# Performance work log

Measured on AMD Instinct MI355X. Metric: run time of the kernel, lower is better.

Reference implementation:

```python
import jax, jax.numpy as jnp
import numpy as np

N = 20000
E = 640000
D = 128


def setup_inputs() -> dict:
    key = jax.random.key(0)
    ks = jax.random.split(key, 8)
    x = jax.random.normal(ks[0], (N, D), dtype=jnp.float32)
    edge_index = jax.random.randint(ks[1], (2, E), 0, N, dtype=jnp.int64)
    s = 1.0 / np.sqrt(D)
    inp = {"x": x, "edge_index": edge_index}
    for i, layer in enumerate([2, 4, 6]):
        inp[f"W{i+1}"] = jax.random.uniform(ks[layer], (D, D), jnp.float32, -s, s)
        inp[f"b{i+1}"] = jax.random.uniform(ks[layer + 1], (D,), jnp.float32, -s, s)
    return inp


def _gcn_layer(x, src, dst, deg_inv, W, b):
    # linear (torch convention: y = x @ W.T + b), W: [out, in]
    xt = x @ W.T + b
    # gather source-node features, scatter-mean onto targets
    msg = xt[src]                                   # [E, D]
    agg = jax.ops.segment_sum(msg, dst, num_segments=N)  # [N, D]
    agg = agg * deg_inv[:, None]                    # mean over incoming edges
    return jax.nn.relu(agg) + xt


def reference(x, edge_index, W1, b1, W2, b2, W3, b3):
    src, dst = edge_index[0], edge_index[1]
    deg = jax.ops.segment_sum(jnp.ones((E,), jnp.float32), dst, num_segments=N)
    deg_inv = jnp.where(deg > 0, 1.0 / jnp.maximum(deg, 1.0), 0.0)
    for W, b in ((W1, b1), (W2, b2), (W3, b3)):
        x = _gcn_layer(x, src, dst, deg_inv, W, b)
    return x
```

## Files before the change

### kernel.cpp

```cpp
#include <hip/hip_runtime.h>

#define DD 128
#define KC 32
#define MT 64
#define ELLC 128
#define NBMAX 320
#define ACAP 2304
#define AEPW 4096

__device__ __forceinline__ unsigned f2bf_rne(float f) {
    unsigned u = __float_as_uint(f);
    u += 0x7fffu + ((u >> 16) & 1u);
    return u >> 16;
}

__device__ __forceinline__ void gemm_body(float Xs[KC][MT + 4], float Ws[KC][DD + 4],
                                          const float* x,
                                          const float* __restrict__ W,
                                          const float* __restrict__ b,
                                          float* xt,
                                          unsigned* __restrict__ xtb, int M, int PS, int blk) {
    const int tid  = threadIdx.x;
    const int cg   = tid & 15;
    const int rg   = tid >> 4;
    const int row0 = blk * MT;

    float acc[4][8];
#pragma unroll
    for (int i = 0; i < 4; ++i)
#pragma unroll
        for (int j = 0; j < 8; ++j) acc[i][j] = 0.0f;

    for (int kc = 0; kc < DD; kc += KC) {
#pragma unroll
        for (int it = 0; it < 2; ++it) {
            int idx = tid + it * 256;
            int r = idx >> 3, kq = idx & 7;
            int gr = row0 + r;
            float4 v = make_float4(0.f, 0.f, 0.f, 0.f);
            if (gr < M) v = *(const float4*)&x[gr * DD + kc + kq * 4];
            Xs[kq * 4 + 0][r] = v.x; Xs[kq * 4 + 1][r] = v.y;
            Xs[kq * 4 + 2][r] = v.z; Xs[kq * 4 + 3][r] = v.w;
        }
#pragma unroll
        for (int it = 0; it < 4; ++it) {
            int idx = tid + it * 256;
            int o = idx >> 3, kq = idx & 7;
            float4 v = *(const float4*)&W[o * DD + kc + kq * 4];
            Ws[kq * 4 + 0][o] = v.x; Ws[kq * 4 + 1][o] = v.y;
            Ws[kq * 4 + 2][o] = v.z; Ws[kq * 4 + 3][o] = v.w;
        }
        __syncthreads();

#pragma unroll 8
        for (int k = 0; k < KC; ++k) {
            float4 xv = *(const float4*)&Xs[k][rg * 4];
            float4 w0 = *(const float4*)&Ws[k][cg * 8];
            float4 w1 = *(const float4*)&Ws[k][cg * 8 + 4];
            float xr[4] = {xv.x, xv.y, xv.z, xv.w};
            float wc[8] = {w0.x, w0.y, w0.z, w0.w, w1.x, w1.y, w1.z, w1.w};
#pragma unroll
            for (int i = 0; i < 4; ++i)
#pragma unroll
                for (int j = 0; j < 8; ++j) acc[i][j] += xr[i] * wc[j];
        }
        __syncthreads();
    }

    float4 b0 = *(const float4*)&b[cg * 8];
    float4 b1 = *(const float4*)&b[cg * 8 + 4];
    float bb[8] = {b0.x, b0.y, b0.z, b0.w, b1.x, b1.y, b1.z, b1.w};
#pragma unroll
    for (int i = 0; i < 4; ++i) {
        int gr = row0 + rg * 4 + i;
        if (gr < M) {
            float v[8];
#pragma unroll
            for (int j = 0; j < 8; ++j) v[j] = acc[i][j] + bb[j];
            *(float4*)&xt[gr * DD + cg * 8]     = make_float4(v[0], v[1], v[2], v[3]);
            *(float4*)&xt[gr * DD + cg * 8 + 4] = make_float4(v[4], v[5], v[6], v[7]);
            uint4 p;
            p.x = f2bf_rne(v[0]) | (f2bf_rne(v[1]) << 16);
            p.y = f2bf_rne(v[2]) | (f2bf_rne(v[3]) << 16);
            p.z = f2bf_rne(v[4]) | (f2bf_rne(v[5]) << 16);
            p.w = f2bf_rne(v[6]) | (f2bf_rne(v[7]) << 16);
            unsigned* xp = xtb + (size_t)(cg >> 3) * ((size_t)PS * 32)
                               + (size_t)gr * 32 + ((cg & 7) << 2);
            *(uint4*)xp = p;
        }
    }
}

__global__ __launch_bounds__(256) void gemm_xwT(const float* x,
                                                const float* __restrict__ W,
                                                const float* __restrict__ b,
                                                float* xt,
                                                unsigned* __restrict__ xtb, int M, int PS) {
    __shared__ float Xs[KC][MT + 4];
    __shared__ float Ws[KC][DD + 4];
    gemm_body(Xs, Ws, x, W, b, xt, xtb, M, PS, blockIdx.x);
}

__global__ __launch_bounds__(256) void gemm1_plus_binA(const float* x,
                                                       const float* __restrict__ W,
                                                       const float* __restrict__ b,
                                                       float* xt,
                                                       unsigned* __restrict__ xtb, int M, int PS,
                                                       const int* __restrict__ src,
                                                       const int* __restrict__ dst,
                                                       int* __restrict__ bucket_count,
                                                       unsigned* __restrict__ bstore,
                                                       int E, int NB, int PA) {
    __shared__ float Xs[KC][MT + 4];
    __shared__ float Ws[KC][DD + 4];
    __shared__ int hist[NBMAX];
    __shared__ int basec[NBMAX];
    __shared__ int cur[NBMAX];

    if ((int)blockIdx.x >= PA) {
        gemm_body(Xs, Ws, x, W, b, xt, xtb, M, PS, blockIdx.x - PA);
        return;
    }

    const int tid = threadIdx.x;
    for (int i = tid; i < NB; i += 256) hist[i] = 0;
    __syncthreads();

    int dv[16], sv[16];
    const int ebase = blockIdx.x * AEPW;
#pragma unroll
    for (int r = 0; r < 4; ++r) {
        int e = ebase + r * 1024 + tid * 4;
        if (e + 4 <= E) {
            int4 d4 = *(const int4*)&dst[e];
            int4 s4 = *(const int4*)&src[e];
            dv[r*4+0] = d4.x; dv[r*4+1] = d4.y; dv[r*4+2] = d4.z; dv[r*4+3] = d4.w;
            sv[r*4+0] = s4.x; sv[r*4+1] = s4.y; sv[r*4+2] = s4.z; sv[r*4+3] = s4.w;
        } else {
#pragma unroll
            for (int q = 0; q < 4; ++q) {
                int ee = e + q;
                if (ee < E) { dv[r*4+q] = dst[ee]; sv[r*4+q] = src[ee]; }
                else        { dv[r*4+q] = -1;      sv[r*4+q] = 0; }
            }
        }
    }
#pragma unroll
    for (int i = 0; i < 16; ++i)
        if (dv[i] >= 0) atomicAdd(&hist[dv[i] >> 6], 1);
    __syncthreads();

    for (int bk = tid; bk < NB; bk += 256) {
        int h = hist[bk];
        basec[bk] = h ? atomicAdd(&bucket_count[bk], h) : 0;
        cur[bk] = 0;
    }
    __syncthreads();

#pragma unroll
    for (int i = 0; i < 16; ++i) {
        if (dv[i] >= 0) {
            int bk = dv[i] >> 6;
            int pos = basec[bk] + atomicAdd(&cur[bk], 1);
            if (pos < ACAP)
                bstore[bk * ACAP + pos] = ((unsigned)(dv[i] & 63) << 16) | (unsigned)sv[i];
        }
    }
}

__global__ __launch_bounds__(256) void ell_build(const unsigned* __restrict__ bstore,
                                                 const int* __restrict__ bucket_count,
                                                 unsigned short* __restrict__ colell,
                                                 int* __restrict__ deg,
                                                 unsigned* __restrict__ xtb,
                                                 int PS, int N) {
    __shared__ int c64[64];
    const int bk = blockIdx.x;
    for (int i = threadIdx.x; i < 64; i += 256) c64[i] = 0;
    __syncthreads();
    int cnt = bucket_count[bk];
    if (cnt > ACAP) cnt = ACAP;
    for (int i = threadIdx.x; i < cnt; i += 256) {
        unsigned code = bstore[bk * ACAP + i];
        int local = (int)(code >> 16);
        int s     = (int)(code & 0xffffu);
        int p = atomicAdd(&c64[local], 1);
        if (p < ELLC)
            colell[((((bk << 6) + local)) << 7) + p] = (unsigned short)s;
    }
    __syncthreads();
    if (threadIdx.x < 64) {
        int node = (bk << 6) + threadIdx.x;
        if (node < N) {
            int d = c64[threadIdx.x];
            deg[node] = d;
            int stored = d < ELLC ? d : ELLC;
            int padded = (stored + 15) & ~15;
            if (padded > ELLC) padded = ELLC;
            unsigned short* row = colell + ((size_t)node << 7);
            for (int p2 = stored; p2 < padded; ++p2) row[p2] = (unsigned short)N;
        }
    }
    if (bk == 0 && threadIdx.x >= 64 && threadIdx.x < 80) {
        int i  = threadIdx.x - 64;
        int pl = i >> 3;
        int j  = i & 7;
        *(uint4*)&xtb[((size_t)pl * PS + (size_t)N) * 32 + (size_t)j * 4] =
            make_uint4(0u, 0u, 0u, 0u);
    }
}

__global__ __launch_bounds__(256) void gcn_aggregate(const uint2* __restrict__ xtb2,
                                                     const float* xt,
                                                     const unsigned short* __restrict__ colell,
                                                     const int* __restrict__ deg,
                                                     float* out, int PS, int N) {
    const int wave  = threadIdx.x >> 6;
    const int lane  = threadIdx.x & 63;
    const int xcd   = blockIdx.x & 7;
    const int plane = xcd >> 2;
    const int widx  = ((blockIdx.x >> 3) << 2) | (xcd & 3);
    const int node  = (widx << 2) | wave;
    if (node >= N) return;
    const int h = lane & 15;
    const int q = lane >> 4;

    const uint2* __restrict__ xl = xtb2 + (size_t)plane * ((size_t)PS << 4) + h;
    const unsigned short* __restrict__ crow = colell + ((size_t)node << 7);
    const int cnt = deg[node];
    const int cl  = cnt < ELLC ? cnt : ELLC;

    float a0 = 0.f, a1 = 0.f, a2 = 0.f, a3 = 0.f;

#define GATH(u_, j_) { int s_ = __shfl(myidx, ((t + (j_)) << 2) | q, 64); \
                       (u_)[j_] = xl[(size_t)s_ << 4]; }
#define UNPK(u_, j_) { a0 += __uint_as_float((u_)[j_].x << 16); \
                       a1 += __uint_as_float((u_)[j_].x & 0xffff0000u); \
                       a2 += __uint_as_float((u_)[j_].y << 16); \
                       a3 += __uint_as_float((u_)[j_].y & 0xffff0000u); }

    for (int base = 0; base < cl; base += 64) {
        const int rem = cl - base;
        const int c = rem < 64 ? rem : 64;
        const int myidx = (int)crow[base + lane];
        const int cq = ((c + 15) >> 4) << 2;
        int t = 0;
        for (; t + 8 <= cq; t += 8) {
            uint2 u[8];
            GATH(u,0) GATH(u,1) GATH(u,2) GATH(u,3)
            GATH(u,4) GATH(u,5) GATH(u,6) GATH(u,7)
            UNPK(u,0) UNPK(u,1) UNPK(u,2) UNPK(u,3)
            UNPK(u,4) UNPK(u,5) UNPK(u,6) UNPK(u,7)
        }
        if (t < cq) {
            uint2 u[4];
            GATH(u,0) GATH(u,1) GATH(u,2) GATH(u,3)
            UNPK(u,0) UNPK(u,1) UNPK(u,2) UNPK(u,3)
        }
    }
#undef GATH
#undef UNPK

    a0 += __shfl_down(a0, 32, 64);
    a1 += __shfl_down(a1, 32, 64);
    a2 += __shfl_down(a2, 32, 64);
    a3 += __shfl_down(a3, 32, 64);
    a0 += __shfl_down(a0, 16, 64);
    a1 += __shfl_down(a1, 16, 64);
    a2 += __shfl_down(a2, 16, 64);
    a3 += __shfl_down(a3, 16, 64);

    if (q == 0) {
        const float di = (cnt > 0) ? (1.0f / (float)cnt) : 0.0f;
        float4 t4 = ((const float4*)xt)[(size_t)node * 32 + plane * 16 + h];
        float4 o;
        o.x = fmaxf(a0 * di, 0.f) + t4.x;
        o.y = fmaxf(a1 * di, 0.f) + t4.y;
        o.z = fmaxf(a2 * di, 0.f) + t4.z;
        o.w = fmaxf(a3 * di, 0.f) + t4.w;
        ((float4*)out)[(size_t)node * 32 + plane * 16 + h] = o;
    }
}

extern "C" void kernel_launch(void* const* d_in, const int* in_sizes, int n_in,
                              void* d_out, int out_size, void* d_ws, size_t ws_size,
                              hipStream_t stream) {
    const float* x  = (const float*)d_in[0];
    const int*   ei = (const int*)d_in[1];
    const float* W1 = (const float*)d_in[2];
    const float* b1 = (const float*)d_in[3];
    const float* W2 = (const float*)d_in[4];
    const float* b2 = (const float*)d_in[5];
    const float* W3 = (const float*)d_in[6];
    const float* b3 = (const float*)d_in[7];

    const int N  = in_sizes[0] / DD;
    const int E  = in_sizes[1] / 2;
    const int PS = N + 1;

    const int* src = ei;
    const int* dst = ei + E;

    const int NB = (N + 63) >> 6;
    const int PA = (E + AEPW - 1) / AEPW;
    const int GB = (N + MT - 1) / MT;
    const int SUP = (N + 15) >> 4;
    const int AGB = SUP * 8;

    char* ws = (char*)d_ws;
    size_t off = 0;
    auto alloc = [&](size_t bytes) {
        void* p = ws + off;
        off += (bytes + 255) & ~(size_t)255;
        return p;
    };
    int*            bucket_count = (int*)alloc((size_t)NB * sizeof(int));
    unsigned*       bstore       = (unsigned*)alloc((size_t)NB * ACAP * sizeof(unsigned));
    unsigned short* colell       = (unsigned short*)alloc((size_t)NB * 64 * ELLC * sizeof(unsigned short));
    int*            deg          = (int*)alloc((size_t)N * sizeof(int));
    unsigned*       xtb          = (unsigned*)alloc((size_t)PS * 256);

    float* xbuf = (float*)d_out;

    hipMemsetAsync(bucket_count, 0, (size_t)NB * sizeof(int), stream);
    gemm1_plus_binA<<<PA + GB, 256, 0, stream>>>(x, W1, b1, xbuf, xtb, N, PS,
                                                 src, dst, bucket_count, bstore, E, NB, PA);
    ell_build<<<NB, 256, 0, stream>>>(bstore, bucket_count, colell, deg, xtb, PS, N);

    gcn_aggregate<<<AGB, 256, 0, stream>>>((const uint2*)xtb, xbuf, colell, deg, xbuf, PS, N);

    gemm_xwT<<<GB, 256, 0, stream>>>(xbuf, W2, b2, xbuf, xtb, N, PS);
    gcn_aggregate<<<AGB, 256, 0, stream>>>((const uint2*)xtb, xbuf, colell, deg, xbuf, PS, N);

    gemm_xwT<<<GB, 256, 0, stream>>>(xbuf, W3, b3, xbuf, xtb, N, PS);
    gcn_aggregate<<<AGB, 256, 0, stream>>>((const uint2*)xtb, xbuf, colell, deg, xbuf, PS, N);
}
```

Before: 213.5 us.

## Use persistent work-queue aggregation with XCC-aware plane assignment and finer padding

Replaces the static-grid aggregation kernel with a persistent kernel of fixed block count. Blocks grab groups of 16 nodes from per-plane atomic counters, first on the feature plane matched to their XCC, then help with the other plane. ELL row padding drops from multiples of 16 to multiples of 4, and a single-step gather tail replaces the 4-wide one, so fewer padding gathers are wasted. This costs atomic contention, two block syncs per chunk and a hardware-register read, and it relies on the XCC id to keep each plane's data local in cache.

```diff
diff --git a/kernel.cpp b/kernel.cpp
--- a/kernel.cpp
+++ b/kernel.cpp
@@ -7,6 +7,8 @@
 #define NBMAX 320
 #define ACAP 2304
 #define AEPW 4096
+#define AGB  1024
+#define QG   16
 
 __device__ __forceinline__ unsigned f2bf_rne(float f) {
     unsigned u = __float_as_uint(f);
@@ -14,14 +16,20 @@
     return u >> 16;
 }
 
-__device__ __forceinline__ void gemm_body(float Xs[KC][MT + 4], float Ws[KC][DD + 4],
+__device__ __forceinline__ int xcc_id() {
+    unsigned v;
+    asm volatile("s_getreg_b32 %0, hwreg(20, 0, 4)" : "=s"(v));
+    return (int)(v & 7u);
+}
+
+__device__ __forceinline__ void gemm_body(float (*Xs)[MT + 4], float (*Ws)[DD + 4],
                                           const float* x,
                                           const float* __restrict__ W,
                                           const float* __restrict__ b,
                                           float* xt,
                                           unsigned* __restrict__ xtb, int M, int PS, int blk) {
     const int tid  = threadIdx.x;
-    const int cg   = tid & 15;
+    const int cg_  = tid & 15;
     const int rg   = tid >> 4;
     const int row0 = blk * MT;
 
@@ -55,8 +63,8 @@
 #pragma unroll 8
         for (int k = 0; k < KC; ++k) {
             float4 xv = *(const float4*)&Xs[k][rg * 4];
-            float4 w0 = *(const float4*)&Ws[k][cg * 8];
-            float4 w1 = *(const float4*)&Ws[k][cg * 8 + 4];
+            float4 w0 = *(const float4*)&Ws[k][cg_ * 8];
+            float4 w1 = *(const float4*)&Ws[k][cg_ * 8 + 4];
             float xr[4] = {xv.x, xv.y, xv.z, xv.w};
             float wc[8] = {w0.x, w0.y, w0.z, w0.w, w1.x, w1.y, w1.z, w1.w};
 #pragma unroll
@@ -67,8 +75,8 @@
         __syncthreads();
     }
 
-    float4 b0 = *(const float4*)&b[cg * 8];
-    float4 b1 = *(const float4*)&b[cg * 8 + 4];
+    float4 b0 = *(const float4*)&b[cg_ * 8];
+    float4 b1 = *(const float4*)&b[cg_ * 8 + 4];
     float bb[8] = {b0.x, b0.y, b0.z, b0.w, b1.x, b1.y, b1.z, b1.w};
 #pragma unroll
     for (int i = 0; i < 4; ++i) {
@@ -77,15 +85,15 @@
             float v[8];
 #pragma unroll
             for (int j = 0; j < 8; ++j) v[j] = acc[i][j] + bb[j];
-            *(float4*)&xt[gr * DD + cg * 8]     = make_float4(v[0], v[1], v[2], v[3]);
-            *(float4*)&xt[gr * DD + cg * 8 + 4] = make_float4(v[4], v[5], v[6], v[7]);
+            *(float4*)&xt[gr * DD + cg_ * 8]     = make_float4(v[0], v[1], v[2], v[3]);
+            *(float4*)&xt[gr * DD + cg_ * 8 + 4] = make_float4(v[4], v[5], v[6], v[7]);
             uint4 p;
             p.x = f2bf_rne(v[0]) | (f2bf_rne(v[1]) << 16);
             p.y = f2bf_rne(v[2]) | (f2bf_rne(v[3]) << 16);
             p.z = f2bf_rne(v[4]) | (f2bf_rne(v[5]) << 16);
             p.w = f2bf_rne(v[6]) | (f2bf_rne(v[7]) << 16);
-            unsigned* xp = xtb + (size_t)(cg >> 3) * ((size_t)PS * 32)
-                               + (size_t)gr * 32 + ((cg & 7) << 2);
+            unsigned* xp = xtb + (size_t)(cg_ >> 3) * ((size_t)PS * 32)
+                               + (size_t)gr * 32 + ((cg_ & 7) << 2);
             *(uint4*)xp = p;
         }
     }
@@ -110,6 +118,7 @@
                                                        const int* __restrict__ dst,
                                                        int* __restrict__ bucket_count,
                                                        unsigned* __restrict__ bstore,
+                                                       int* __restrict__ qc,
                                                        int E, int NB, int PA) {
     __shared__ float Xs[KC][MT + 4];
     __shared__ float Ws[KC][DD + 4];
@@ -123,6 +132,7 @@
     }
 
     const int tid = threadIdx.x;
+    if (blockIdx.x == 0 && tid < 6) qc[tid] = 0;
     for (int i = tid; i < NB; i += 256) hist[i] = 0;
     __syncthreads();
 
@@ -195,7 +205,7 @@
             int d = c64[threadIdx.x];
             deg[node] = d;
             int stored = d < ELLC ? d : ELLC;
-            int padded = (stored + 15) & ~15;
+            int padded = (stored + 3) & ~3;
             if (padded > ELLC) padded = ELLC;
             unsigned short* row = colell + ((size_t)node << 7);
             for (int p2 = stored; p2 < padded; ++p2) row[p2] = (unsigned short)N;
@@ -210,18 +220,10 @@
     }
 }
 
-__global__ __launch_bounds__(256) void gcn_aggregate(const uint2* __restrict__ xtb2,
-                                                     const float* xt,
-                                                     const unsigned short* __restrict__ colell,
-                                                     const int* __restrict__ deg,
-                                                     float* out, int PS, int N) {
-    const int wave  = threadIdx.x >> 6;
-    const int lane  = threadIdx.x & 63;
-    const int xcd   = blockIdx.x & 7;
-    const int plane = xcd >> 2;
-    const int widx  = ((blockIdx.x >> 3) << 2) | (xcd & 3);
-    const int node  = (widx << 2) | wave;
-    if (node >= N) return;
+__device__ __forceinline__ void agg_one(const uint2* __restrict__ xtb2, const float* xt,
+                                        const unsigned short* __restrict__ colell,
+                                        const int* __restrict__ deg, float* out,
+                                        int PS, int node, int plane, int lane) {
     const int h = lane & 15;
     const int q = lane >> 4;
 
@@ -243,7 +245,7 @@
         const int rem = cl - base;
         const int c = rem < 64 ? rem : 64;
         const int myidx = (int)crow[base + lane];
-        const int cq = ((c + 15) >> 4) << 2;
+        const int cq = (c + 3) >> 2;
         int t = 0;
         for (; t + 8 <= cq; t += 8) {
             uint2 u[8];
@@ -252,10 +254,9 @@
             UNPK(u,0) UNPK(u,1) UNPK(u,2) UNPK(u,3)
             UNPK(u,4) UNPK(u,5) UNPK(u,6) UNPK(u,7)
         }
-        if (t < cq) {
-            uint2 u[4];
-            GATH(u,0) GATH(u,1) GATH(u,2) GATH(u,3)
-            UNPK(u,0) UNPK(u,1) UNPK(u,2) UNPK(u,3)
+        for (; t < cq; ++t) {
+            uint2 u1[1];
+            GATH(u1,0) UNPK(u1,0)
         }
     }
 #undef GATH
@@ -279,6 +280,37 @@
         o.z = fmaxf(a2 * di, 0.f) + t4.z;
         o.w = fmaxf(a3 * di, 0.f) + t4.w;
         ((float4*)out)[(size_t)node * 32 + plane * 16 + h] = o;
+    }
+}
+
+__global__ __launch_bounds__(256) void gcn_aggregate_q(const uint2* __restrict__ xtb2,
+                                                       const float* xt,
+                                                       const unsigned short* __restrict__ colell,
+                                                       const int* __restrict__ deg,
+                                                       float* out,
+                                                       int* __restrict__ qc,
+                                                       int PS, int N) {
+    __shared__ int sbase;
+    const int wave = threadIdx.x >> 6;
+    const int lane = threadIdx.x & 63;
+    const int myplane = (xcc_id() >> 2) & 1;
+
+    for (int pass = 0; pass < 2; ++pass) {
+        const int plane = myplane ^ pass;
+        int* q = qc + plane;
+        for (;;) {
+            if (threadIdx.x == 0) sbase = atomicAdd(q, QG);
+            __syncthreads();
+            const int base = sbase;
+            __syncthreads();
+            if (base >= N) break;
+#pragma unroll
+            for (int r = 0; r < QG / 4; ++r) {
+                int node = base + (r << 2) + wave;
+                if (node < N)
+                    agg_one(xtb2, xt, colell, deg, out, PS, node, plane, lane);
+            }
+        }
     }
 }
 
@@ -304,8 +336,6 @@
     const int NB = (N + 63) >> 6;
     const int PA = (E + AEPW - 1) / AEPW;
     const int GB = (N + MT - 1) / MT;
-    const int SUP = (N + 15) >> 4;
-    const int AGB = SUP * 8;
 
     char* ws = (char*)d_ws;
     size_t off = 0;
@@ -319,19 +349,23 @@
     unsigned short* colell       = (unsigned short*)alloc((size_t)NB * 64 * ELLC * sizeof(unsigned short));
     int*            deg          = (int*)alloc((size_t)N * sizeof(int));
     unsigned*       xtb          = (unsigned*)alloc((size_t)PS * 256);
+    int*            qc           = (int*)alloc(6 * sizeof(int));
 
     float* xbuf = (float*)d_out;
 
     hipMemsetAsync(bucket_count, 0, (size_t)NB * sizeof(int), stream);
     gemm1_plus_binA<<<PA + GB, 256, 0, stream>>>(x, W1, b1, xbuf, xtb, N, PS,
-                                                 src, dst, bucket_count, bstore, E, NB, PA);
+                                                 src, dst, bucket_count, bstore, qc, E, NB, PA);
     ell_build<<<NB, 256, 0, stream>>>(bstore, bucket_count, colell, deg, xtb, PS, N);
 
-    gcn_aggregate<<<AGB, 256, 0, stream>>>((const uint2*)xtb, xbuf, colell, deg, xbuf, PS, N);
+    gcn_aggregate_q<<<AGB, 256, 0, stream>>>((const uint2*)xtb, xbuf, colell, deg, xbuf,
+                                             qc + 0, PS, N);
 
     gemm_xwT<<<GB, 256, 0, stream>>>(xbuf, W2, b2, xbuf, xtb, N, PS);
-    gcn_aggregate<<<AGB, 256, 0, stream>>>((const uint2*)xtb, xbuf, colell, deg, xbuf, PS, N);
+    gcn_aggregate_q<<<AGB, 256, 0, stream>>>((const uint2*)xtb, xbuf, colell, deg, xbuf,
+                                             qc + 2, PS, N);
 
     gemm_xwT<<<GB, 256, 0, stream>>>(xbuf, W3, b3, xbuf, xtb, N, PS);
-    gcn_aggregate<<<AGB, 256, 0, stream>>>((const uint2*)xtb, xbuf, colell, deg, xbuf, PS, N);
-}
+    gcn_aggregate_q<<<AGB, 256, 0, stream>>>((const uint2*)xtb, xbuf, colell, deg, xbuf,
+                                             qc + 4, PS, N);
+}
```

New measurement: 347.1 us. 62.6% more time.

## Process both feature planes per wave and shrink ELL padding to four

Applied to the files above, without the earlier changes.

The aggregate kernel now handles both 64-feature bf16 planes of a node in one wave, not splitting planes across XCD-mapped blocks. This halves the block count and reuses each shuffled neighbor index for two gathers. Row padding drops from 16 to 4 entries, and a scalar tail loop replaces the 4-wide remainder, so fewer dummy gathers are issued. The trade-off is losing the XCD-based plane locality for L2, which could make the gathers miss cache more often.

```diff
diff --git a/kernel.cpp b/kernel.cpp
--- a/kernel.cpp
+++ b/kernel.cpp
@@ -14,14 +14,14 @@
     return u >> 16;
 }
 
-__device__ __forceinline__ void gemm_body(float Xs[KC][MT + 4], float Ws[KC][DD + 4],
+__device__ __forceinline__ void gemm_body(float (*Xs)[MT + 4], float (*Ws)[DD + 4],
                                           const float* x,
                                           const float* __restrict__ W,
                                           const float* __restrict__ b,
                                           float* xt,
                                           unsigned* __restrict__ xtb, int M, int PS, int blk) {
     const int tid  = threadIdx.x;
-    const int cg   = tid & 15;
+    const int cg_  = tid & 15;
     const int rg   = tid >> 4;
     const int row0 = blk * MT;
 
@@ -55,8 +55,8 @@
 #pragma unroll 8
         for (int k = 0; k < KC; ++k) {
             float4 xv = *(const float4*)&Xs[k][rg * 4];
-            float4 w0 = *(const float4*)&Ws[k][cg * 8];
-            float4 w1 = *(const float4*)&Ws[k][cg * 8 + 4];
+            float4 w0 = *(const float4*)&Ws[k][cg_ * 8];
+            float4 w1 = *(const float4*)&Ws[k][cg_ * 8 + 4];
             float xr[4] = {xv.x, xv.y, xv.z, xv.w};
             float wc[8] = {w0.x, w0.y, w0.z, w0.w, w1.x, w1.y, w1.z, w1.w};
 #pragma unroll
@@ -67,8 +67,8 @@
         __syncthreads();
     }
 
-    float4 b0 = *(const float4*)&b[cg * 8];
-    float4 b1 = *(const float4*)&b[cg * 8 + 4];
+    float4 b0 = *(const float4*)&b[cg_ * 8];
+    float4 b1 = *(const float4*)&b[cg_ * 8 + 4];
     float bb[8] = {b0.x, b0.y, b0.z, b0.w, b1.x, b1.y, b1.z, b1.w};
 #pragma unroll
     for (int i = 0; i < 4; ++i) {
@@ -77,15 +77,15 @@
             float v[8];
 #pragma unroll
             for (int j = 0; j < 8; ++j) v[j] = acc[i][j] + bb[j];
-            *(float4*)&xt[gr * DD + cg * 8]     = make_float4(v[0], v[1], v[2], v[3]);
-            *(float4*)&xt[gr * DD + cg * 8 + 4] = make_float4(v[4], v[5], v[6], v[7]);
+            *(float4*)&xt[gr * DD + cg_ * 8]     = make_float4(v[0], v[1], v[2], v[3]);
+            *(float4*)&xt[gr * DD + cg_ * 8 + 4] = make_float4(v[4], v[5], v[6], v[7]);
             uint4 p;
             p.x = f2bf_rne(v[0]) | (f2bf_rne(v[1]) << 16);
             p.y = f2bf_rne(v[2]) | (f2bf_rne(v[3]) << 16);
             p.z = f2bf_rne(v[4]) | (f2bf_rne(v[5]) << 16);
             p.w = f2bf_rne(v[6]) | (f2bf_rne(v[7]) << 16);
-            unsigned* xp = xtb + (size_t)(cg >> 3) * ((size_t)PS * 32)
-                               + (size_t)gr * 32 + ((cg & 7) << 2);
+            unsigned* xp = xtb + (size_t)(cg_ >> 3) * ((size_t)PS * 32)
+                               + (size_t)gr * 32 + ((cg_ & 7) << 2);
             *(uint4*)xp = p;
         }
     }
@@ -195,7 +195,7 @@
             int d = c64[threadIdx.x];
             deg[node] = d;
             int stored = d < ELLC ? d : ELLC;
-            int padded = (stored + 15) & ~15;
+            int padded = (stored + 3) & ~3;
             if (padded > ELLC) padded = ELLC;
             unsigned short* row = colell + ((size_t)node << 7);
             for (int p2 = stored; p2 < padded; ++p2) row[p2] = (unsigned short)N;
@@ -215,70 +215,80 @@
                                                      const unsigned short* __restrict__ colell,
                                                      const int* __restrict__ deg,
                                                      float* out, int PS, int N) {
-    const int wave  = threadIdx.x >> 6;
-    const int lane  = threadIdx.x & 63;
-    const int xcd   = blockIdx.x & 7;
-    const int plane = xcd >> 2;
-    const int widx  = ((blockIdx.x >> 3) << 2) | (xcd & 3);
-    const int node  = (widx << 2) | wave;
+    const int wave = threadIdx.x >> 6;
+    const int lane = threadIdx.x & 63;
+    const int node = (int)blockIdx.x * 4 + wave;
     if (node >= N) return;
     const int h = lane & 15;
     const int q = lane >> 4;
 
-    const uint2* __restrict__ xl = xtb2 + (size_t)plane * ((size_t)PS << 4) + h;
+    const uint2* __restrict__ xl0 = xtb2 + h;
+    const uint2* __restrict__ xl1 = xtb2 + ((size_t)PS << 4) + h;
     const unsigned short* __restrict__ crow = colell + ((size_t)node << 7);
     const int cnt = deg[node];
     const int cl  = cnt < ELLC ? cnt : ELLC;
 
     float a0 = 0.f, a1 = 0.f, a2 = 0.f, a3 = 0.f;
-
-#define GATH(u_, j_) { int s_ = __shfl(myidx, ((t + (j_)) << 2) | q, 64); \
-                       (u_)[j_] = xl[(size_t)s_ << 4]; }
-#define UNPK(u_, j_) { a0 += __uint_as_float((u_)[j_].x << 16); \
-                       a1 += __uint_as_float((u_)[j_].x & 0xffff0000u); \
-                       a2 += __uint_as_float((u_)[j_].y << 16); \
-                       a3 += __uint_as_float((u_)[j_].y & 0xffff0000u); }
+    float a4 = 0.f, a5 = 0.f, a6 = 0.f, a7 = 0.f;
+
+#define GATH2(j_) { int s_ = __shfl(myidx, ((t + (j_)) << 2) | q, 64); \
+                    u0[j_] = xl0[(size_t)s_ << 4]; \
+                    u1[j_] = xl1[(size_t)s_ << 4]; }
+#define UNPK2(j_) { a0 += __uint_as_float(u0[j_].x << 16); \
+                    a1 += __uint_as_float(u0[j_].x & 0xffff0000u); \
+                    a2 += __uint_as_float(u0[j_].y << 16); \
+                    a3 += __uint_as_float(u0[j_].y & 0xffff0000u); \
+                    a4 += __uint_as_float(u1[j_].x << 16); \
+                    a5 += __uint_as_float(u1[j_].x & 0xffff0000u); \
+                    a6 += __uint_as_float(u1[j_].y << 16); \
+                    a7 += __uint_as_float(u1[j_].y & 0xffff0000u); }
 
     for (int base = 0; base < cl; base += 64) {
         const int rem = cl - base;
         const int c = rem < 64 ? rem : 64;
         const int myidx = (int)crow[base + lane];
-        const int cq = ((c + 15) >> 4) << 2;
+        const int cq = (c + 3) >> 2;
         int t = 0;
         for (; t + 8 <= cq; t += 8) {
-            uint2 u[8];
-            GATH(u,0) GATH(u,1) GATH(u,2) GATH(u,3)
-            GATH(u,4) GATH(u,5) GATH(u,6) GATH(u,7)
-            UNPK(u,0) UNPK(u,1) UNPK(u,2) UNPK(u,3)
-            UNPK(u,4) UNPK(u,5) UNPK(u,6) UNPK(u,7)
-        }
-        if (t < cq) {
-            uint2 u[4];
-            GATH(u,0) GATH(u,1) GATH(u,2) GATH(u,3)
-            UNPK(u,0) UNPK(u,1) UNPK(u,2) UNPK(u,3)
-        }
-    }
-#undef GATH
-#undef UNPK
-
-    a0 += __shfl_down(a0, 32, 64);
-    a1 += __shfl_down(a1, 32, 64);
-    a2 += __shfl_down(a2, 32, 64);
-    a3 += __shfl_down(a3, 32, 64);
-    a0 += __shfl_down(a0, 16, 64);
-    a1 += __shfl_down(a1, 16, 64);
-    a2 += __shfl_down(a2, 16, 64);
-    a3 += __shfl_down(a3, 16, 64);
+            uint2 u0[8], u1[8];
+            GATH2(0) GATH2(1) GATH2(2) GATH2(3)
+            GATH2(4) GATH2(5) GATH2(6) GATH2(7)
+            UNPK2(0) UNPK2(1) UNPK2(2) UNPK2(3)
+            UNPK2(4) UNPK2(5) UNPK2(6) UNPK2(7)
+        }
+        for (; t < cq; ++t) {
+            uint2 u0[1], u1[1];
+            GATH2(0)
+            UNPK2(0)
+        }
+    }
+#undef GATH2
+#undef UNPK2
+
+    a0 += __shfl_down(a0, 32, 64); a1 += __shfl_down(a1, 32, 64);
+    a2 += __shfl_down(a2, 32, 64); a3 += __shfl_down(a3, 32, 64);
+    a4 += __shfl_down(a4, 32, 64); a5 += __shfl_down(a5, 32, 64);
+    a6 += __shfl_down(a6, 32, 64); a7 += __shfl_down(a7, 32, 64);
+    a0 += __shfl_down(a0, 16, 64); a1 += __shfl_down(a1, 16, 64);
+    a2 += __shfl_down(a2, 16, 64); a3 += __shfl_down(a3, 16, 64);
+    a4 += __shfl_down(a4, 16, 64); a5 += __shfl_down(a5, 16, 64);
+    a6 += __shfl_down(a6, 16, 64); a7 += __shfl_down(a7, 16, 64);
 
     if (q == 0) {
         const float di = (cnt > 0) ? (1.0f / (float)cnt) : 0.0f;
-        float4 t4 = ((const float4*)xt)[(size_t)node * 32 + plane * 16 + h];
-        float4 o;
-        o.x = fmaxf(a0 * di, 0.f) + t4.x;
-        o.y = fmaxf(a1 * di, 0.f) + t4.y;
-        o.z = fmaxf(a2 * di, 0.f) + t4.z;
-        o.w = fmaxf(a3 * di, 0.f) + t4.w;
-        ((float4*)out)[(size_t)node * 32 + plane * 16 + h] = o;
+        float4 tA = ((const float4*)xt)[(size_t)node * 32 + h];
+        float4 tB = ((const float4*)xt)[(size_t)node * 32 + 16 + h];
+        float4 oA, oB;
+        oA.x = fmaxf(a0 * di, 0.f) + tA.x;
+        oA.y = fmaxf(a1 * di, 0.f) + tA.y;
+        oA.z = fmaxf(a2 * di, 0.f) + tA.z;
+        oA.w = fmaxf(a3 * di, 0.f) + tA.w;
+        oB.x = fmaxf(a4 * di, 0.f) + tB.x;
+        oB.y = fmaxf(a5 * di, 0.f) + tB.y;
+        oB.z = fmaxf(a6 * di, 0.f) + tB.z;
+        oB.w = fmaxf(a7 * di, 0.f) + tB.w;
+        ((float4*)out)[(size_t)node * 32 + h]      = oA;
+        ((float4*)out)[(size_t)node * 32 + 16 + h] = oB;
     }
 }
 
@@ -304,8 +314,7 @@
     const int NB = (N + 63) >> 6;
     const int PA = (E + AEPW - 1) / AEPW;
     const int GB = (N + MT - 1) / MT;
-    const int SUP = (N + 15) >> 4;
-    const int AGB = SUP * 8;
+    const int AB = (N + 3) / 4;
 
     char* ws = (char*)d_ws;
     size_t off = 0;
@@ -327,11 +336,11 @@
                                                  src, dst, bucket_count, bstore, E, NB, PA);
     ell_build<<<NB, 256, 0, stream>>>(bstore, bucket_count, colell, deg, xtb, PS, N);
 
-    gcn_aggregate<<<AGB, 256, 0, stream>>>((const uint2*)xtb, xbuf, colell, deg, xbuf, PS, N);
+    gcn_aggregate<<<AB, 256, 0, stream>>>((const uint2*)xtb, xbuf, colell, deg, xbuf, PS, N);
 
     gemm_xwT<<<GB, 256, 0, stream>>>(xbuf, W2, b2, xbuf, xtb, N, PS);
-    gcn_aggregate<<<AGB, 256, 0, stream>>>((const uint2*)xtb, xbuf, colell, deg, xbuf, PS, N);
+    gcn_aggregate<<<AB, 256, 0, stream>>>((const uint2*)xtb, xbuf, colell, deg, xbuf, PS, N);
 
     gemm_xwT<<<GB, 256, 0, stream>>>(xbuf, W3, b3, xbuf, xtb, N, PS);
-    gcn_aggregate<<<AGB, 256, 0, stream>>>((const uint2*)xtb, xbuf, colell, deg, xbuf, PS, N);
-}
+    gcn_aggregate<<<AB, 256, 0, stream>>>((const uint2*)xtb, xbuf, colell, deg, xbuf, PS, N);
+}
```

After: 226.8 us. +6.2%, slower.
